# Kernel optimization log

Measured on AMD Instinct MI355X. Metric: run time of the kernel, lower is better.

The kernel has to match this reference:

```python
import jax, jax.numpy as jnp
import numpy as np


def setup_inputs() -> dict:
    key = jax.random.key(0)
    k0, k1, k2, k3, k4 = jax.random.split(key, 5)
    B, C, H, W = 32, 64, 128, 128
    return {
        "x": jax.random.normal(k0, (B, C, H, W), jnp.float32),
        "w1d": jax.random.normal(k1, (64,), jnp.float32) * 0.1,   # Conv1d(1,1,k=64,s=64) weight
        "b1d": jax.random.normal(k2, (1,), jnp.float32) * 0.1,    # Conv1d bias
        "wdw": jax.random.normal(k3, (C, 1, 9, 9), jnp.float32) * 0.05,  # depthwise Conv2d weight (OIHW, groups=C)
        "bdw": jax.random.normal(k4, (C,), jnp.float32) * 0.05,   # depthwise Conv2d bias
    }


def _cov_linear(x, w1d, b1d):
    # Batched torch.cov over channels, followed by Conv1d(1,1,k=64,stride=64)
    B, C, H, W = x.shape
    f = x.reshape(B, C, H * W)
    f = f - f.mean(axis=-1, keepdims=True)
    cov = jnp.einsum('bcn,bdn->bcd', f, f) / (H * W - 1)  # [B, C, C]
    # Conv1d with kernel=stride=64 on the flattened C*C vector == segmented dot
    seg = cov.reshape(B, (C * C) // 64, 64)               # [B, C, 64] since C == 64
    return seg @ w1d + b1d                                # [B, C]


def reference(x, w1d, b1d, wdw, bdw):
    C = x.shape[1]
    c = _cov_linear(x, w1d, b1d)
    # 9x9 depthwise conv, padding=4 (same spatial size)
    y = jax.lax.conv_general_dilated(
        x, wdw, window_strides=(1, 1), padding=[(4, 4), (4, 4)],
        dimension_numbers=('NCHW', 'OIHW', 'NCHW'), feature_group_count=C)
    y = y + bdw[None, :, None, None]
    c_ = _cov_linear(y, w1d, b1d)
    raise_ch = jax.nn.softmax(c_ - c, axis=1)             # softmax over channel scores
    att = jax.nn.sigmoid(c_ * (1.0 + raise_ch))           # [B, C]
    return y * att[:, :, None, None]
```

## Files before the change

kernel.cpp:

```cpp
#include <hip/hip_runtime.h>

#define NSP 16384
#define CCH 64
#define BATCH 32
#define SPLIT 8
#define CPB (CCH / SPLIT)

#define LW 160
#define LH 40
#define LDSF (LW * LH)
#define NQ (LDSF / 4)
#define NISS 7

__device__ __forceinline__ void gload_lds16(const float* g, float* l) {
    __builtin_amdgcn_global_load_lds(
        (const __attribute__((address_space(1))) void*)g,
        (__attribute__((address_space(3))) void*)l,
        16, 0, 0);
}

__device__ __forceinline__ int swq(int q) { return q ^ ((q >> 3) & 7); }

__device__ __forceinline__ unsigned short f2bf(float f) {
    unsigned u = __float_as_uint(f);
    u += 0x7fffu + ((u >> 16) & 1u);
    return (unsigned short)(u >> 16);
}
__device__ __forceinline__ float bflo(unsigned u) { return __uint_as_float(u << 16); }
__device__ __forceinline__ float bfhi(unsigned u) { return __uint_as_float(u & 0xffff0000u); }

template<int YBF>
__global__ __launch_bounds__(256, 3) void conv_kernel(
    const float* __restrict__ x, const float* __restrict__ wdw,
    const float* __restrict__ bdw, const float* __restrict__ w1d,
    const float* __restrict__ zpad,
    float* __restrict__ yf, unsigned short* __restrict__ yb,
    float* __restrict__ ty_parts)
{
    const int tile = blockIdx.x;
    const int b    = blockIdx.y;
    const int sp   = blockIdx.z;
    const int tile_ry = tile * 32;
    const int tid = threadIdx.x;
    const int tx = tid & 15, ty = tid >> 4;
    const int c0 = tx * 8, r0 = ty * 2;
    const int cbase = sp * CPB;

    __shared__ float bufs[2][LDSF];

    int soff[NISS]; unsigned okm = 0;
    #pragma unroll
    for (int r = 0; r < NISS; ++r) {
        int q = tid + 256 * r;
        int lrow = q / 40, qcl = q - lrow * 40;
        int gq = swq(qcl);
        int gr = tile_ry - 4 + lrow;
        int gc = gq * 4 - 4;
        soff[r] = gr * 128 + gc;
        if (q < NQ && (unsigned)gr < 128u && gq >= 1 && gq <= 32) okm |= 1u << r;
    }

    int rb[4];
    #pragma unroll
    for (int j = 0; j < 4; ++j) rb[j] = r0 * LW + swq(2 * tx + j) * 4;

    const float* xb = x + (size_t)b * CCH * NSP;

#define STAGE(cc, dst) do {                                               \
        const float* plane_ = xb + (size_t)(cc) * NSP;                    \
        _Pragma("unroll")                                                 \
        for (int r_ = 0; r_ < NISS; ++r_) {                               \
            int q_ = tid + 256 * r_;                                      \
            if (q_ < NQ) {                                                \
                const float* g_ = ((okm >> r_) & 1u) ? plane_ + soff[r_]  \
                                                     : zpad;              \
                gload_lds16(g_, &(dst)[4 * q_]);                          \
            }                                                             \
        }                                                                 \
    } while (0)

    STAGE(cbase, bufs[0]);

    float tya[2][8] = {};
    __syncthreads();

    for (int k = 0; k < CPB; ++k) {
        const int c = cbase + k;
        if (k + 1 < CPB) STAGE(c + 1, bufs[(k + 1) & 1]);

        const float* cb = bufs[k & 1];
        const float* wc = wdw + c * 81;
        float acc[2][8] = {};
        #pragma unroll
        for (int ir = 0; ir < 10; ++ir) {
            float4 f0 = *(const float4*)(cb + rb[0] + ir * LW);
            float4 f1 = *(const float4*)(cb + rb[1] + ir * LW);
            float4 f2 = *(const float4*)(cb + rb[2] + ir * LW);
            float4 f3 = *(const float4*)(cb + rb[3] + ir * LW);
            float v[16] = {f0.x, f0.y, f0.z, f0.w, f1.x, f1.y, f1.z, f1.w,
                           f2.x, f2.y, f2.z, f2.w, f3.x, f3.y, f3.z, f3.w};
            #pragma unroll
            for (int o = 0; o < 2; ++o) {
                int tv = ir - o;
                if (tv >= 0 && tv <= 8) {
                    #pragma unroll
                    for (int kx = 0; kx < 9; ++kx) {
                        float w = wc[tv * 9 + kx];
                        #pragma unroll
                        for (int q = 0; q < 8; ++q) acc[o][q] += w * v[kx + q];
                    }
                }
            }
        }

        const float bias = bdw[c];
        const float w1c  = w1d[c];
        const size_t ybase = (size_t)(b * CCH + c) * NSP + (tile_ry + r0) * 128 + c0;
        #pragma unroll
        for (int o = 0; o < 2; ++o) {
            float yv[8];
            #pragma unroll
            for (int q = 0; q < 8; ++q) {
                yv[q] = acc[o][q] + bias;
                tya[o][q] += w1c * yv[q];
            }
            if (YBF) {
                uint4 s;
                s.x = (unsigned)f2bf(yv[0]) | ((unsigned)f2bf(yv[1]) << 16);
                s.y = (unsigned)f2bf(yv[2]) | ((unsigned)f2bf(yv[3]) << 16);
                s.z = (unsigned)f2bf(yv[4]) | ((unsigned)f2bf(yv[5]) << 16);
                s.w = (unsigned)f2bf(yv[6]) | ((unsigned)f2bf(yv[7]) << 16);
                *(uint4*)(yb + ybase + o * 128) = s;
            } else {
                *(float4*)(yf + ybase + o * 128) =
                    make_float4(yv[0], yv[1], yv[2], yv[3]);
                *(float4*)(yf + ybase + o * 128 + 4) =
                    make_float4(yv[4], yv[5], yv[6], yv[7]);
            }
        }
        __syncthreads();
    }
#undef STAGE

    const size_t tb = ((size_t)sp * BATCH + b) * NSP + (tile_ry + r0) * 128 + c0;
    float* typ = ty_parts + tb;
    #pragma unroll
    for (int o = 0; o < 2; ++o) {
        *(float4*)(typ + o * 128)     = make_float4(tya[o][0], tya[o][1], tya[o][2], tya[o][3]);
        *(float4*)(typ + o * 128 + 4) = make_float4(tya[o][4], tya[o][5], tya[o][6], tya[o][7]);
    }
}

__global__ __launch_bounds__(256) void tcomp_kernel(
    const float4* __restrict__ x4, const float4* __restrict__ parts,
    const float* __restrict__ w1d,
    float4* __restrict__ t_x, float4* __restrict__ t_y)
{
    const int b = blockIdx.y;
    const int p = blockIdx.x * 256 + threadIdx.x;
    const float4* xb = x4 + (size_t)b * CCH * (NSP / 4) + p;
    float4 ax = make_float4(0.f, 0.f, 0.f, 0.f);
    #pragma unroll 8
    for (int c = 0; c < CCH; ++c) {
        float w = w1d[c];
        float4 v = xb[(size_t)c * (NSP / 4)];
        ax.x += w * v.x; ax.y += w * v.y; ax.z += w * v.z; ax.w += w * v.w;
    }
    float4 ay = make_float4(0.f, 0.f, 0.f, 0.f);
    const float4* pb = parts + (size_t)b * (NSP / 4) + p;
    #pragma unroll
    for (int r = 0; r < SPLIT; ++r) {
        float4 v = pb[(size_t)r * BATCH * (NSP / 4)];
        ay.x += v.x; ay.y += v.y; ay.z += v.z; ay.w += v.w;
    }
    t_x[(size_t)b * (NSP / 4) + p] = ax;
    t_y[(size_t)b * (NSP / 4) + p] = ay;
}

template<int YBF>
__global__ __launch_bounds__(256) void dot_kernel(
    const float* __restrict__ x, const float* __restrict__ yf,
    const unsigned short* __restrict__ yb,
    const float* __restrict__ t_x, const float* __restrict__ t_y,
    float* __restrict__ dot_x, float* __restrict__ dot_y,
    float* __restrict__ S_x, float* __restrict__ S_y)
{
    const int bc = blockIdx.x;
    const int b  = bc >> 6;
    const int tid = threadIdx.x;
    const float4* xr  = (const float4*)(x   + (size_t)bc * NSP);
    const float4* txr = (const float4*)(t_x + (size_t)b * NSP);
    const float4* tyr = (const float4*)(t_y + (size_t)b * NSP);
    float dx = 0.f, dy = 0.f, sx = 0.f, sy = 0.f;
    if (YBF) {
        const uint4* yr = (const uint4*)(yb + (size_t)bc * NSP);
        for (int i = tid; i < NSP / 8; i += 256) {
            float4 x0 = xr[2 * i], x1 = xr[2 * i + 1];
            float4 t0 = txr[2 * i], t1 = txr[2 * i + 1];
            float4 u0 = tyr[2 * i], u1 = tyr[2 * i + 1];
            uint4 yv = yr[i];
            float y0 = bflo(yv.x), y1 = bfhi(yv.x), y2 = bflo(yv.y), y3 = bfhi(yv.y);
            float y4 = bflo(yv.z), y5 = bfhi(yv.z), y6 = bflo(yv.w), y7 = bfhi(yv.w);
            dx += x0.x * t0.x + x0.y * t0.y + x0.z * t0.z + x0.w * t0.w
                + x1.x * t1.x + x1.y * t1.y + x1.z * t1.z + x1.w * t1.w;
            sx += x0.x + x0.y + x0.z + x0.w + x1.x + x1.y + x1.z + x1.w;
            dy += y0 * u0.x + y1 * u0.y + y2 * u0.z + y3 * u0.w
                + y4 * u1.x + y5 * u1.y + y6 * u1.z + y7 * u1.w;
            sy += y0 + y1 + y2 + y3 + y4 + y5 + y6 + y7;
        }
    } else {
        const float4* yr = (const float4*)(yf + (size_t)bc * NSP);
        for (int i = tid; i < NSP / 4; i += 256) {
            float4 xv = xr[i], tv = txr[i];
            float4 yv = yr[i], uv = tyr[i];
            dx += xv.x * tv.x + xv.y * tv.y + xv.z * tv.z + xv.w * tv.w;
            sx += xv.x + xv.y + xv.z + xv.w;
            dy += yv.x * uv.x + yv.y * uv.y + yv.z * uv.z + yv.w * uv.w;
            sy += yv.x + yv.y + yv.z + yv.w;
        }
    }
    #pragma unroll
    for (int off = 32; off > 0; off >>= 1) {
        dx += __shfl_down(dx, off);
        dy += __shfl_down(dy, off);
        sx += __shfl_down(sx, off);
        sy += __shfl_down(sy, off);
    }
    __shared__ float red[16];
    const int wid = tid >> 6;
    if ((tid & 63) == 0) {
        red[wid * 4]     = dx; red[wid * 4 + 1] = dy;
        red[wid * 4 + 2] = sx; red[wid * 4 + 3] = sy;
    }
    __syncthreads();
    if (tid == 0) {
        dot_x[bc] = red[0] + red[4] + red[8]  + red[12];
        dot_y[bc] = red[1] + red[5] + red[9]  + red[13];
        S_x[bc]   = red[2] + red[6] + red[10] + red[14];
        S_y[bc]   = red[3] + red[7] + red[11] + red[15];
    }
}

__global__ __launch_bounds__(64) void att_kernel(
    const float* __restrict__ S_x, const float* __restrict__ S_y,
    const float* __restrict__ dot_x, const float* __restrict__ dot_y,
    const float* __restrict__ w1d, const float* __restrict__ b1d,
    float* __restrict__ att)
{
    const int b = blockIdx.x;
    const int c = threadIdx.x;
    const float sx = S_x[b * CCH + c];
    const float sy = S_y[b * CCH + c];
    const float w  = w1d[c];
    float tsx = w * sx, tsy = w * sy;
    #pragma unroll
    for (int off = 32; off > 0; off >>= 1) {
        tsx += __shfl_xor(tsx, off);
        tsy += __shfl_xor(tsy, off);
    }
    const float inv_n  = 1.f / 16384.f;
    const float inv_n1 = 1.f / 16383.f;
    const float bb = b1d[0];
    float cxv = (dot_x[b * CCH + c] - sx * inv_n * tsx) * inv_n1 + bb;
    float cyv = (dot_y[b * CCH + c] - sy * inv_n * tsy) * inv_n1 + bb;
    float d = cyv - cxv;
    float m = d;
    #pragma unroll
    for (int off = 32; off > 0; off >>= 1) m = fmaxf(m, __shfl_xor(m, off));
    float e = __expf(d - m);
    float s = e;
    #pragma unroll
    for (int off = 32; off > 0; off >>= 1) s += __shfl_xor(s, off);
    float r = e / s;
    float a = cyv * (1.f + r);
    att[b * CCH + c] = 1.f / (1.f + __expf(-a));
}

template<int YBF>
__global__ __launch_bounds__(256) void scale_kernel(
    const unsigned short* __restrict__ yb, float* __restrict__ out,
    const float* __restrict__ att)
{
    const size_t total8 = (size_t)BATCH * CCH * NSP / 8;
    size_t i = (size_t)blockIdx.x * blockDim.x + threadIdx.x;
    const size_t stride = (size_t)gridDim.x * blockDim.x;
    if (YBF) {
        for (; i < total8; i += stride) {
            uint4 y = ((const uint4*)yb)[i];
            float a = att[(i * 8) >> 14];
            float4 o0 = make_float4(bflo(y.x) * a, bfhi(y.x) * a,
                                    bflo(y.y) * a, bfhi(y.y) * a);
            float4 o1 = make_float4(bflo(y.z) * a, bfhi(y.z) * a,
                                    bflo(y.w) * a, bfhi(y.w) * a);
            ((float4*)out)[2 * i]     = o0;
            ((float4*)out)[2 * i + 1] = o1;
        }
    } else {
        for (; i < total8; i += stride) {
            float a = att[(i * 8) >> 14];
            float4 v0 = ((const float4*)out)[2 * i];
            float4 v1 = ((const float4*)out)[2 * i + 1];
            v0.x *= a; v0.y *= a; v0.z *= a; v0.w *= a;
            v1.x *= a; v1.y *= a; v1.z *= a; v1.w *= a;
            ((float4*)out)[2 * i]     = v0;
            ((float4*)out)[2 * i + 1] = v1;
        }
    }
}

extern "C" void kernel_launch(void* const* d_in, const int* in_sizes, int n_in,
                              void* d_out, int out_size, void* d_ws, size_t ws_size,
                              hipStream_t stream) {
    const float* x   = (const float*)d_in[0];
    const float* w1d = (const float*)d_in[1];
    const float* b1d = (const float*)d_in[2];
    const float* wdw = (const float*)d_in[3];
    const float* bdw = (const float*)d_in[4];
    float* out = (float*)d_out;
    float* fw  = (float*)d_ws;

    const size_t PARTSY = (size_t)SPLIT * BATCH * NSP;
    float* ty_parts = fw;
    float* t_x      = ty_parts + PARTSY;
    float* t_y      = t_x + (size_t)BATCH * NSP;
    float* S_x      = t_y + (size_t)BATCH * NSP;
    float* S_y      = S_x + 2048;
    float* dot_x    = S_y + 2048;
    float* dot_y    = dot_x + 2048;
    float* att      = dot_y + 2048;
    float* zpad     = att + 2048;
    float* fend     = zpad + 64;
    size_t fbytes   = (size_t)((char*)fend - (char*)fw);
    fbytes = (fbytes + 255) & ~(size_t)255;
    unsigned short* yb = (unsigned short*)((char*)d_ws + fbytes);
    const size_t yb_bytes = (size_t)BATCH * CCH * NSP * 2;

    const bool ybf = (ws_size >= fbytes + yb_bytes);

    hipMemsetAsync(zpad, 0, 64 * sizeof(float), stream);

    if (ybf) {
        conv_kernel<1><<<dim3(4, BATCH, SPLIT), 256, 0, stream>>>(
            x, wdw, bdw, w1d, zpad, out, yb, ty_parts);
        tcomp_kernel<<<dim3(NSP / 4 / 256, BATCH), 256, 0, stream>>>(
            (const float4*)x, (const float4*)ty_parts, w1d,
            (float4*)t_x, (float4*)t_y);
        dot_kernel<1><<<2048, 256, 0, stream>>>(x, out, yb, t_x, t_y,
                                                dot_x, dot_y, S_x, S_y);
        att_kernel<<<BATCH, 64, 0, stream>>>(S_x, S_y, dot_x, dot_y, w1d, b1d, att);
        scale_kernel<1><<<2048, 256, 0, stream>>>(yb, out, att);
    } else {
        conv_kernel<0><<<dim3(4, BATCH, SPLIT), 256, 0, stream>>>(
            x, wdw, bdw, w1d, zpad, out, yb, ty_parts);
        tcomp_kernel<<<dim3(NSP / 4 / 256, BATCH), 256, 0, stream>>>(
            (const float4*)x, (const float4*)ty_parts, w1d,
            (float4*)t_x, (float4*)t_y);
        dot_kernel<0><<<2048, 256, 0, stream>>>(x, out, yb, t_x, t_y,
                                                dot_x, dot_y, S_x, S_y);
        att_kernel<<<BATCH, 64, 0, stream>>>(S_x, S_y, dot_x, dot_y, w1d, b1d, att);
        scale_kernel<0><<<2048, 256, 0, stream>>>(yb, out, att);
    }
}
```

Measured before the change: 188.1 us.

## Fuse t_x/t_y reductions into depthwise conv kernel via atomics, drop tcomp kernel

The conv kernel now also accumulates the w1d-weighted channel sum of x, reading the centre taps already staged in LDS, alongside the y sum. Both partial sums are added into t_x/t_y with atomicAdd across the 8 channel splits instead of writing per-split partials. This removes the separate tcomp kernel, its 64-channel re-read of x and the partial buffer traffic, at the cost of a memset plus scattered scalar float atomics. The LDS row pitch changes from 160 to 164 floats, which also changes the staging index math.

Result: slower. 333.7 us (+77.4%).

```diff
diff --git a/kernel.cpp b/kernel.cpp
--- a/kernel.cpp
+++ b/kernel.cpp
@@ -6,7 +6,7 @@
 #define SPLIT 8
 #define CPB (CCH / SPLIT)
 
-#define LW 160
+#define LW 164
 #define LH 40
 #define LDSF (LW * LH)
 #define NQ (LDSF / 4)
@@ -35,7 +35,7 @@
     const float* __restrict__ bdw, const float* __restrict__ w1d,
     const float* __restrict__ zpad,
     float* __restrict__ yf, unsigned short* __restrict__ yb,
-    float* __restrict__ ty_parts)
+    float* __restrict__ t_x, float* __restrict__ t_y)
 {
     const int tile = blockIdx.x;
     const int b    = blockIdx.y;
@@ -52,7 +52,7 @@
     #pragma unroll
     for (int r = 0; r < NISS; ++r) {
         int q = tid + 256 * r;
-        int lrow = q / 40, qcl = q - lrow * 40;
+        int lrow = q / 41, qcl = q - lrow * 41;
         int gq = swq(qcl);
         int gr = tile_ry - 4 + lrow;
         int gc = gq * 4 - 4;
@@ -81,6 +81,7 @@
 
     STAGE(cbase, bufs[0]);
 
+    float txa[2][8] = {};
     float tya[2][8] = {};
     __syncthreads();
 
@@ -91,6 +92,7 @@
         const float* cb = bufs[k & 1];
         const float* wc = wdw + c * 81;
         float acc[2][8] = {};
+        float cx[2][8];
         #pragma unroll
         for (int ir = 0; ir < 10; ++ir) {
             float4 f0 = *(const float4*)(cb + rb[0] + ir * LW);
@@ -99,6 +101,14 @@
             float4 f3 = *(const float4*)(cb + rb[3] + ir * LW);
             float v[16] = {f0.x, f0.y, f0.z, f0.w, f1.x, f1.y, f1.z, f1.w,
                            f2.x, f2.y, f2.z, f2.w, f3.x, f3.y, f3.z, f3.w};
+            if (ir == 4) {
+                #pragma unroll
+                for (int q = 0; q < 8; ++q) cx[0][q] = v[q + 4];
+            }
+            if (ir == 5) {
+                #pragma unroll
+                for (int q = 0; q < 8; ++q) cx[1][q] = v[q + 4];
+            }
             #pragma unroll
             for (int o = 0; o < 2; ++o) {
                 int tv = ir - o;
@@ -122,6 +132,7 @@
             #pragma unroll
             for (int q = 0; q < 8; ++q) {
                 yv[q] = acc[o][q] + bias;
+                txa[o][q] += w1c * cx[o][q];
                 tya[o][q] += w1c * yv[q];
             }
             if (YBF) {
@@ -142,39 +153,17 @@
     }
 #undef STAGE
 
-    const size_t tb = ((size_t)sp * BATCH + b) * NSP + (tile_ry + r0) * 128 + c0;
-    float* typ = ty_parts + tb;
+    const size_t tb = (size_t)b * NSP + (tile_ry + r0) * 128 + c0;
+    float* txp = t_x + tb;
+    float* typ = t_y + tb;
     #pragma unroll
     for (int o = 0; o < 2; ++o) {
-        *(float4*)(typ + o * 128)     = make_float4(tya[o][0], tya[o][1], tya[o][2], tya[o][3]);
-        *(float4*)(typ + o * 128 + 4) = make_float4(tya[o][4], tya[o][5], tya[o][6], tya[o][7]);
-    }
-}
-
-__global__ __launch_bounds__(256) void tcomp_kernel(
-    const float4* __restrict__ x4, const float4* __restrict__ parts,
-    const float* __restrict__ w1d,
-    float4* __restrict__ t_x, float4* __restrict__ t_y)
-{
-    const int b = blockIdx.y;
-    const int p = blockIdx.x * 256 + threadIdx.x;
-    const float4* xb = x4 + (size_t)b * CCH * (NSP / 4) + p;
-    float4 ax = make_float4(0.f, 0.f, 0.f, 0.f);
-    #pragma unroll 8
-    for (int c = 0; c < CCH; ++c) {
-        float w = w1d[c];
-        float4 v = xb[(size_t)c * (NSP / 4)];
-        ax.x += w * v.x; ax.y += w * v.y; ax.z += w * v.z; ax.w += w * v.w;
-    }
-    float4 ay = make_float4(0.f, 0.f, 0.f, 0.f);
-    const float4* pb = parts + (size_t)b * (NSP / 4) + p;
-    #pragma unroll
-    for (int r = 0; r < SPLIT; ++r) {
-        float4 v = pb[(size_t)r * BATCH * (NSP / 4)];
-        ay.x += v.x; ay.y += v.y; ay.z += v.z; ay.w += v.w;
-    }
-    t_x[(size_t)b * (NSP / 4) + p] = ax;
-    t_y[(size_t)b * (NSP / 4) + p] = ay;
+        #pragma unroll
+        for (int q = 0; q < 8; ++q) {
+            atomicAdd(txp + o * 128 + q, txa[o][q]);
+            atomicAdd(typ + o * 128 + q, tya[o][q]);
+        }
+    }
 }
 
 template<int YBF>
@@ -319,9 +308,7 @@
     float* out = (float*)d_out;
     float* fw  = (float*)d_ws;
 
-    const size_t PARTSY = (size_t)SPLIT * BATCH * NSP;
-    float* ty_parts = fw;
-    float* t_x      = ty_parts + PARTSY;
+    float* t_x      = fw;
     float* t_y      = t_x + (size_t)BATCH * NSP;
     float* S_x      = t_y + (size_t)BATCH * NSP;
     float* S_y      = S_x + 2048;
@@ -337,24 +324,19 @@
 
     const bool ybf = (ws_size >= fbytes + yb_bytes);
 
+    hipMemsetAsync(t_x, 0, (size_t)2 * BATCH * NSP * sizeof(float), stream);
     hipMemsetAsync(zpad, 0, 64 * sizeof(float), stream);
 
     if (ybf) {
         conv_kernel<1><<<dim3(4, BATCH, SPLIT), 256, 0, stream>>>(
-            x, wdw, bdw, w1d, zpad, out, yb, ty_parts);
-        tcomp_kernel<<<dim3(NSP / 4 / 256, BATCH), 256, 0, stream>>>(
-            (const float4*)x, (const float4*)ty_parts, w1d,
-            (float4*)t_x, (float4*)t_y);
+            x, wdw, bdw, w1d, zpad, out, yb, t_x, t_y);
         dot_kernel<1><<<2048, 256, 0, stream>>>(x, out, yb, t_x, t_y,
                                                 dot_x, dot_y, S_x, S_y);
         att_kernel<<<BATCH, 64, 0, stream>>>(S_x, S_y, dot_x, dot_y, w1d, b1d, att);
         scale_kernel<1><<<2048, 256, 0, stream>>>(yb, out, att);
     } else {
         conv_kernel<0><<<dim3(4, BATCH, SPLIT), 256, 0, stream>>>(
-            x, wdw, bdw, w1d, zpad, out, yb, ty_parts);
-        tcomp_kernel<<<dim3(NSP / 4 / 256, BATCH), 256, 0, stream>>>(
-            (const float4*)x, (const float4*)ty_parts, w1d,
-            (float4*)t_x, (float4*)t_y);
+            x, wdw, bdw, w1d, zpad, out, yb, t_x, t_y);
         dot_kernel<0><<<2048, 256, 0, stream>>>(x, out, yb, t_x, t_y,
                                                 dot_x, dot_y, S_x, S_y);
         att_kernel<<<BATCH, 64, 0, stream>>>(S_x, S_y, dot_x, dot_y, w1d, b1d, att);
```
